# Kernel optimization log

Hardware: AMD Instinct MI355X
Metric: run time of the kernel (lower is better)

The kernel has to match this reference:

```python
import jax, jax.numpy as jnp
import numpy as np

B, N, C, H = 2, 1024, 768, 12
D = C // H
SCALE = D ** -0.5


def setup_inputs() -> dict:
    key = jax.random.key(0)
    ks = jax.random.split(key, 6)
    s = 1.0 / np.sqrt(C)
    return {
        "x": jax.random.normal(ks[0], (B, N, C), jnp.float32),
        "Wqkv": jax.random.normal(ks[1], (3 * C, C), jnp.float32) * s,   # qkv_bias=False
        "Wa": jax.random.normal(ks[2], (H, C), jnp.float32) * s,        # selective gate Linear(dim, H)
        "ba": jnp.zeros((H,), jnp.float32),
        "Wproj": jax.random.normal(ks[3], (C, C), jnp.float32) * s,
        "bproj": jnp.zeros((C,), jnp.float32),
    }


def _silu_shifted(z):
    # silu(x) + 0.5, L2-normalized over head dim (silunorm=True)
    r = jax.nn.silu(z) + 0.5
    return r / jnp.linalg.norm(r, axis=-1, keepdims=True)


def _forward(x, Wqkv, Wa, ba, Wproj, bproj):
    qkv = (x @ Wqkv.T).reshape(B, N, 3, H, D).transpose(2, 0, 3, 1, 4)  # [3,B,H,N,D]
    q = _silu_shifted(qkv[0])
    k = _silu_shifted(qkv[1])
    v = qkv[2]

    # selective forget gates: a = 1 - sigmoid(Linear(x)); torch.tensor(...) detaches -> stop_gradient
    a = jax.lax.stop_gradient(1.0 - jax.nn.sigmoid(x @ Wa.T + ba)).transpose(0, 2, 1)  # [B,H,N]
    # drop first token's gate, prepend 1 (as in the module)
    a = jnp.concatenate([jnp.ones_like(a[..., :1]), a[..., 1:]], axis=-1)

    # Causal_Mask_Selective(log(a)):
    #   A_for[i,j]  = prod_{t=j..i-1} a[t]   (j <= i)
    #   A_back[i,j] = prod_{t=i+1..j} a[t]   (j >= i)
    #   M = A_for + A_back - I
    c = jnp.cumsum(jnp.log(a), axis=-1)
    c = jnp.concatenate([jnp.zeros_like(c[..., :1]), c], axis=-1)  # [B,H,N+1], c[m] = sum log a[0..m-1]
    tri = jnp.tril(jnp.ones((N, N), bool))
    d_for = c[..., :N, None] - c[..., None, :N]      # c[i]-c[j]
    d_back = c[..., None, 1:] - c[..., 1:, None]     # c[j+1]-c[i+1]
    A_for = jnp.where(tri, jnp.exp(jnp.where(tri, d_for, 0.0)), 0.0)
    A_back = jnp.where(tri.T, jnp.exp(jnp.where(tri.T, d_back, 0.0)), 0.0)
    M = A_for + A_back - jnp.eye(N, dtype=x.dtype)

    attn = jnp.einsum('bhid,bhjd->bhij', q, k) * SCALE * M
    attn = attn / (attn.sum(axis=-1, keepdims=True) + 1e-6)  # sum-normalization, NOT softmax
    out = jnp.einsum('bhij,bhjd->bhid', attn, v).transpose(0, 2, 1, 3).reshape(B, N, C)
    return out @ Wproj.T + bproj


def reference(x, Wqkv, Wa, ba, Wproj, bproj):
    return _forward(x, Wqkv, Wa, ba, Wproj, bproj)
```

## Files before the change

### kernel.cpp

```cpp
#include <hip/hip_runtime.h>
#include <hip/hip_bf16.h>

#define BB 2
#define NN 1024
#define CC 768
#define HH 12
#define DD 64
#define SCALE_F 0.125f

typedef __attribute__((ext_vector_type(8))) __bf16 bf16x8;
typedef __attribute__((ext_vector_type(8))) unsigned short u16x8;
typedef __attribute__((ext_vector_type(4))) unsigned short u16x4;
typedef __attribute__((ext_vector_type(4))) float f32x4;

static __device__ __forceinline__ bf16x8 as_bf16x8(u16x8 v) {
  return __builtin_bit_cast(bf16x8, v);
}
static __device__ __forceinline__ unsigned short bf16u(float f) {
  __hip_bfloat16 h = __float2bfloat16(f);
  return __builtin_bit_cast(unsigned short, h);
}
static __device__ __forceinline__ float bf2f(unsigned short u) {
  unsigned int x = ((unsigned int)u) << 16;
  return __builtin_bit_cast(float, x);
}
static __device__ __forceinline__ void gload16(const void* g, void* l) {
  __builtin_amdgcn_global_load_lds(
      (const __attribute__((address_space(1))) unsigned int*)g,
      (__attribute__((address_space(3))) unsigned int*)l, 16, 0, 0);
}

__global__ __launch_bounds__(256) void packgate(
    const float* __restrict__ x, const float* __restrict__ Wa,
    const float* __restrict__ ba, float* __restrict__ loga,
    unsigned short* __restrict__ xb, int n0,
    const float* __restrict__ Wqkv, unsigned short* __restrict__ wqkvb, int n1,
    const float* __restrict__ Wproj, unsigned short* __restrict__ wprojb,
    int n2) {
  __shared__ float was[HH][CC];
  if (blockIdx.x < 512) {
    for (int i = threadIdx.x; i < HH * CC; i += 256)
      was[i / CC][i % CC] = Wa[i];
    __syncthreads();
    const int w = threadIdx.x >> 6, lane = threadIdx.x & 63;
    const int row = blockIdx.x * 4 + w;
    const int b = row >> 10, n = row & 1023;
    const float* xr = x + (size_t)row * CC;
    float xf[12];
#pragma unroll
    for (int j = 0; j < 12; j++) xf[j] = xr[lane + 64 * j];
    float myacc = 0.f;
#pragma unroll
    for (int h = 0; h < HH; h++) {
      float a = 0.f;
#pragma unroll
      for (int j = 0; j < 12; j++) a += xf[j] * was[h][lane + 64 * j];
#pragma unroll
      for (int off = 32; off >= 1; off >>= 1) a += __shfl_xor(a, off, 64);
      if (lane == h) myacc = a;
    }
    if (lane < HH) {
      float acc = myacc + ba[lane];
      float a = 1.f - 1.f / (1.f + __expf(-acc));
      float la = (n == 0) ? 0.f : log2f(a);
      loga[(b * HH + lane) * NN + n] = la;
    }
  } else {
    int i = (blockIdx.x - 512) * 256 + threadIdx.x;
    const float* s;
    unsigned short* d;
    if (i < n0) {
      s = x; d = xb;
    } else if (i < n0 + n1) {
      i -= n0; s = Wqkv; d = wqkvb;
    } else {
      i -= n0 + n1;
      if (i >= n2) return;
      s = Wproj; d = wprojb;
    }
    float4 v = ((const float4*)s)[i];
    u16x4 u = {bf16u(v.x), bf16u(v.y), bf16u(v.z), bf16u(v.w)};
    *(u16x4*)&d[i * 4] = u;
  }
}

template <int BM, int BN, bool BF16OUT>
__global__ __launch_bounds__(256) void gemm_mfma(
    const unsigned short* __restrict__ A, const unsigned short* __restrict__ W,
    const float* __restrict__ bias, void* __restrict__ outv,
    int M, int Nc, int K) {
  __shared__ unsigned short As[2][BM * 64];
  __shared__ unsigned short Ws[2][BN * 64];
  constexpr int FM = BM / 32, FN = BN / 32;
  const int row0 = blockIdx.y * BM;
  const int col0 = blockIdx.x * BN;
  const int t = threadIdx.x;
  const int w = t >> 6, lane = t & 63;
  const int lrow = lane & 15, lgrp = lane >> 4;
  const int wr = w >> 1, wc = w & 1;

  f32x4 acc[FM][FN] = {};

  auto STAGE = [&](int buf, int k0) {
#pragma unroll
    for (int i = 0; i < BM * 8 / 256; i++) {
      int idx = i * 256 + t;
      int row = idx >> 3, sl = (idx & 7) ^ (row & 7);
      gload16(A + (size_t)(row0 + row) * K + k0 + sl * 8, &As[buf][idx * 8]);
    }
#pragma unroll
    for (int i = 0; i < BN * 8 / 256; i++) {
      int idx = i * 256 + t;
      int row = idx >> 3, sl = (idx & 7) ^ (row & 7);
      gload16(W + (size_t)(col0 + row) * K + k0 + sl * 8, &Ws[buf][idx * 8]);
    }
  };

  const int NT = K / 64;
  STAGE(0, 0);
  __syncthreads();

  for (int tt = 0; tt < NT; tt++) {
    const int cur = tt & 1;
    if (tt + 1 < NT) STAGE(cur ^ 1, (tt + 1) * 64);

    bf16x8 af[FM][2], bf[FN][2];
#pragma unroll
    for (int m = 0; m < FM; m++) {
      int row = wr * (BM / 2) + m * 16 + lrow;
      const u16x8* p = (const u16x8*)&As[cur][row * 64];
#pragma unroll
      for (int hk = 0; hk < 2; hk++)
        af[m][hk] = as_bf16x8(p[(hk * 4 + lgrp) ^ (row & 7)]);
    }
#pragma unroll
    for (int n = 0; n < FN; n++) {
      int row = wc * (BN / 2) + n * 16 + lrow;
      const u16x8* p = (const u16x8*)&Ws[cur][row * 64];
#pragma unroll
      for (int hk = 0; hk < 2; hk++)
        bf[n][hk] = as_bf16x8(p[(hk * 4 + lgrp) ^ (row & 7)]);
    }
#pragma unroll
    for (int m = 0; m < FM; m++)
#pragma unroll
      for (int n = 0; n < FN; n++) {
        acc[m][n] = __builtin_amdgcn_mfma_f32_16x16x32_bf16(
            af[m][0], bf[n][0], acc[m][n], 0, 0, 0);
        acc[m][n] = __builtin_amdgcn_mfma_f32_16x16x32_bf16(
            af[m][1], bf[n][1], acc[m][n], 0, 0, 0);
      }
    __syncthreads();
  }

#pragma unroll
  for (int n = 0; n < FN; n++) {
    int col = col0 + wc * (BN / 2) + n * 16 + lrow;
    float bb = (!BF16OUT && bias) ? bias[col] : 0.f;
#pragma unroll
    for (int m = 0; m < FM; m++) {
      int rbase = row0 + wr * (BM / 2) + m * 16 + lgrp * 4;
#pragma unroll
      for (int r = 0; r < 4; r++) {
        float v = acc[m][n][r] + bb;
        if (BF16OUT)
          ((unsigned short*)outv)[(size_t)(rbase + r) * Nc + col] = bf16u(v);
        else
          ((float*)outv)[(size_t)(rbase + r) * Nc + col] = v;
      }
    }
  }
}

__global__ __launch_bounds__(256) void packscan(
    const unsigned short* __restrict__ qkvb, unsigned short* __restrict__ qp,
    unsigned short* __restrict__ kp, unsigned short* __restrict__ vt,
    const float* __restrict__ loga, float* __restrict__ c) {
  __shared__ unsigned short tile[64][65];
  if (blockIdx.x < 12288) {
    const int wid = (blockIdx.x * 256 + threadIdx.x) >> 6;
    const int lane = threadIdx.x & 63;
    int s = wid & 1;
    int rest = wid >> 1;
    int h = rest % HH;
    int n = (rest / HH) % NN;
    int b = rest / (HH * NN);
    float z = bf2f(qkvb[(((size_t)(b * NN + n) * 3 + s) * CC) + h * DD + lane]);
    float sig = 1.f / (1.f + __expf(-z));
    float r = z * sig + 0.5f;
    float ss = r * r;
#pragma unroll
    for (int off = 32; off >= 1; off >>= 1) ss += __shfl_xor(ss, off, 64);
    r *= rsqrtf(ss);
    unsigned short* dst = s ? kp : qp;
    dst[((size_t)(b * HH + h) * NN + n) * DD + lane] = bf16u(r);
  } else if (blockIdx.x < 12672) {
    const int blk = blockIdx.x - 12288;
    const int nt = blk & 15;
    const int bh = blk >> 4;
    const int b = bh / HH, h = bh % HH;
    const int n0 = nt * 64;
    const int t = threadIdx.x;
#pragma unroll
    for (int rep = 0; rep < 16; rep++) {
      int idx = rep * 256 + t;
      int nl = idx >> 6, d = idx & 63;
      tile[d][nl] =
          qkvb[((size_t)(b * NN + n0 + nl) * 3 + 2) * CC + h * DD + d];
    }
    __syncthreads();
#pragma unroll
    for (int rep = 0; rep < 16; rep++) {
      int idx = rep * 256 + t;
      int d = idx >> 6, nl = idx & 63;
      vt[((size_t)bh * DD + d) * NN + n0 + nl] = tile[d][nl];
    }
  } else if (threadIdx.x < 64) {
    const int bh = blockIdx.x - 12672;
    const int lane = threadIdx.x;
    const float4* s4 = (const float4*)(loga + (size_t)bh * NN + lane * 16);
    float v[16];
#pragma unroll
    for (int q = 0; q < 4; q++) {
      float4 tv = s4[q];
      v[q * 4 + 0] = tv.x; v[q * 4 + 1] = tv.y;
      v[q * 4 + 2] = tv.z; v[q * 4 + 3] = tv.w;
    }
    float run = 0.f;
#pragma unroll
    for (int e = 0; e < 16; e++) { run += v[e]; v[e] = run; }
    float tot = run;
#pragma unroll
    for (int off = 1; off < 64; off <<= 1) {
      float nb = __shfl_up(tot, off, 64);
      if (lane >= off) tot += nb;
    }
    float excl = tot - run;
    float* dst = c + (size_t)bh * (NN + 1);
    if (lane == 0) dst[0] = 0.f;
#pragma unroll
    for (int e = 0; e < 16; e++) dst[1 + lane * 16 + e] = v[e] + excl;
  }
}

__global__ __launch_bounds__(256) void attn_mfma(
    const unsigned short* __restrict__ qp, const unsigned short* __restrict__ kp,
    const unsigned short* __restrict__ vt, const float* __restrict__ cbuf,
    unsigned short* __restrict__ attnout) {
  __shared__ unsigned short Ks[2][64 * 64];
  __shared__ unsigned short Vs[2][64 * 64];
  __shared__ unsigned short Aw[4][16 * 64];
  __shared__ float Cw[2][64][17];
  __shared__ float Rw[2][64][5];

  const int qt2 = blockIdx.x & 31;
  const int bh = blockIdx.x >> 5;
  const int b = bh / HH, h = bh % HH;
  const int qrow0 = qt2 * 32;
  const int w = threadIdx.x >> 6;
  const int lane = threadIdx.x & 63;
  const int lrow = lane & 15;
  const int lgrp = lane >> 4;
  const int wq = w & 1;
  const int js = w >> 1;

  bf16x8 qaf[2];
  {
    const u16x8* qrow_p = (const u16x8*)(qp +
        ((size_t)bh * NN + qrow0 + wq * 16 + lrow) * DD);
#pragma unroll
    for (int hk = 0; hk < 2; hk++) qaf[hk] = as_bf16x8(qrow_p[hk * 4 + lgrp]);
  }

  const float* cbh = cbuf + (size_t)bh * (NN + 1);
  float ci[4], ci1[4];
  const int ibase = qrow0 + wq * 16 + lgrp * 4;
#pragma unroll
  for (int r = 0; r < 4; r++) {
    ci[r] = cbh[ibase + r];
    ci1[r] = cbh[ibase + r + 1];
  }

  f32x4 oacc[4] = {};
  float rs[4] = {0.f, 0.f, 0.f, 0.f};

  unsigned short* ksf = &Ks[0][0];
  unsigned short* vsf = &Vs[0][0];

  for (int t = 0; t < 8; t++) {
#pragma unroll
    for (int rep = 0; rep < 4; rep++) {
      int idx = rep * 256 + threadIdx.x;
      int buf = idx >> 9, row = (idx >> 3) & 63;
      int sl = (idx & 7) ^ (row & 7);
      int j0s = (buf * 8 + t) * 64;
      gload16(kp + ((size_t)bh * NN + j0s + row) * DD + sl * 8, ksf + idx * 8);
      gload16(vt + ((size_t)bh * DD + row) * NN + j0s + sl * 8, vsf + idx * 8);
    }
    __syncthreads();

    const int j0 = (js * 8 + t) * 64;

#pragma unroll
    for (int ct = 0; ct < 4; ct++) {
      const int jl = ct * 16 + lrow;
      const int j = j0 + jl;
      f32x4 s = {};
      const u16x8* krow_p = (const u16x8*)&Ks[js][jl * 64];
#pragma unroll
      for (int hk = 0; hk < 2; hk++) {
        bf16x8 kf = as_bf16x8(krow_p[(hk * 4 + lgrp) ^ (jl & 7)]);
        s = __builtin_amdgcn_mfma_f32_16x16x32_bf16(qaf[hk], kf, s, 0, 0, 0);
      }
      const float cj = cbh[j], cj1 = cbh[j + 1];
#pragma unroll
      for (int r = 0; r < 4; r++) {
        const int gi = ibase + r;
        float m = (gi > j) ? exp2f(ci[r] - cj)
                 : (gi < j) ? exp2f(cj1 - ci1[r]) : 1.0f;
        float av = s[r] * SCALE_F * m;
        rs[r] += av;
        int rowa = lgrp * 4 + r;
        Aw[w][rowa * 64 + (jl ^ ((rowa & 7) << 3))] = bf16u(av);
      }
    }

#pragma unroll
    for (int jh = 0; jh < 2; jh++) {
      const u16x8* arow_p = (const u16x8*)&Aw[w][lrow * 64];
      bf16x8 af = as_bf16x8(arow_p[(jh * 4 + lgrp) ^ (lrow & 7)]);
#pragma unroll
      for (int dt = 0; dt < 4; dt++) {
        const int dd = dt * 16 + lrow;
        const u16x8* vrow_p = (const u16x8*)&Vs[js][dd * 64];
        bf16x8 vf = as_bf16x8(vrow_p[(jh * 4 + lgrp) ^ (dd & 7)]);
        oacc[dt] =
            __builtin_amdgcn_mfma_f32_16x16x32_bf16(af, vf, oacc[dt], 0, 0, 0);
      }
    }
    __syncthreads();
  }

#pragma unroll
  for (int r = 0; r < 4; r++) {
#pragma unroll
    for (int off = 1; off <= 8; off <<= 1) rs[r] += __shfl_xor(rs[r], off, 64);
  }

  if (w >= 2) {
#pragma unroll
    for (int dt = 0; dt < 4; dt++)
#pragma unroll
      for (int r = 0; r < 4; r++) Cw[w - 2][lane][dt * 4 + r] = oacc[dt][r];
#pragma unroll
    for (int r = 0; r < 4; r++) Rw[w - 2][lane][r] = rs[r];
  }
  __syncthreads();
  if (w < 2) {
#pragma unroll
    for (int r = 0; r < 4; r++) {
      rs[r] += Rw[w][lane][r];
      rs[r] = 1.f / (rs[r] + 1e-6f);
    }
#pragma unroll
    for (int dt = 0; dt < 4; dt++) {
#pragma unroll
      for (int r = 0; r < 4; r++) {
        const int gi = ibase + r;
        float val = (oacc[dt][r] + Cw[w][lane][dt * 4 + r]) * rs[r];
        attnout[((size_t)b * NN + gi) * CC + h * DD + dt * 16 + lrow] =
            bf16u(val);
      }
    }
  }
}

extern "C" void kernel_launch(void* const* d_in, const int* in_sizes, int n_in,
                              void* d_out, int out_size, void* d_ws,
                              size_t ws_size, hipStream_t stream) {
  const float* x = (const float*)d_in[0];
  const float* Wqkv = (const float*)d_in[1];
  const float* Wa = (const float*)d_in[2];
  const float* ba = (const float*)d_in[3];
  const float* Wproj = (const float*)d_in[4];
  const float* bproj = (const float*)d_in[5];
  float* out = (float*)d_out;

  unsigned short* qkvb = (unsigned short*)d_ws;
  float* loga = (float*)(qkvb + (size_t)BB * NN * 3 * CC);
  float* cbuf = loga + (size_t)BB * HH * NN;
  unsigned short* qp = (unsigned short*)(cbuf + (size_t)BB * HH * (NN + 1));
  unsigned short* kp = qp + (size_t)BB * HH * NN * DD;
  unsigned short* vt = kp + (size_t)BB * HH * NN * DD;
  unsigned short* xb = vt + (size_t)BB * HH * NN * DD;
  unsigned short* wqkvb = xb + (size_t)BB * NN * CC;
  unsigned short* wprojb = wqkvb + (size_t)3 * CC * CC;
  unsigned short* attnoutb = qkvb;

  const int n0 = BB * NN * CC / 4, n1 = 3 * CC * CC / 4, n2 = CC * CC / 4;

  packgate<<<512 + (n0 + n1 + n2 + 255) / 256, 256, 0, stream>>>(
      x, Wa, ba, loga, xb, n0, Wqkv, wqkvb, n1, Wproj, wprojb, n2);
  {
    dim3 grid(3 * CC / 128, BB * NN / 64);
    gemm_mfma<64, 128, true><<<grid, 256, 0, stream>>>(
        xb, wqkvb, nullptr, qkvb, BB * NN, 3 * CC, CC);
  }
  packscan<<<12696, 256, 0, stream>>>(qkvb, qp, kp, vt, loga, cbuf);
  attn_mfma<<<BB * HH * (NN / 32), 256, 0, stream>>>(qp, kp, vt, cbuf,
                                                     attnoutb);
  {
    dim3 grid(CC / 64, BB * NN / 64);
    gemm_mfma<64, 64, false><<<grid, 256, 0, stream>>>(
        attnoutb, wprojb, bproj, out, BB * NN, CC, CC);
  }
}
```

Measured before the change: 146.3 us.

## Fuse silu-norm and V transpose into QKV GEMM epilogue, scan in attention

Removes the separate packscan kernel. The QKV GEMM epilogue now applies the shifted-SiLU and L2 normalization to Q/K, using a cross-lane shuffle over head-dim columns, and writes V transposed directly. The cumulative log-gate scan moves into each attention block and is stored in shared memory, with LDS regions aliased to fit. This drops one launch and a full bf16 qkv round trip through global memory. In exchange the GEMM epilogue does strided scattered stores and every attention block recomputes the scan redundantly.

Result: faster. 128.7 us (-12.0%).

```diff
diff --git a/kernel.cpp b/kernel.cpp
--- a/kernel.cpp
+++ b/kernel.cpp
@@ -19,10 +19,6 @@
 static __device__ __forceinline__ unsigned short bf16u(float f) {
   __hip_bfloat16 h = __float2bfloat16(f);
   return __builtin_bit_cast(unsigned short, h);
-}
-static __device__ __forceinline__ float bf2f(unsigned short u) {
-  unsigned int x = ((unsigned int)u) << 16;
-  return __builtin_bit_cast(float, x);
 }
 static __device__ __forceinline__ void gload16(const void* g, void* l) {
   __builtin_amdgcn_global_load_lds(
@@ -84,11 +80,12 @@
   }
 }
 
-template <int BM, int BN, bool BF16OUT>
+template <int BM, int BN, int EPI>
 __global__ __launch_bounds__(256) void gemm_mfma(
     const unsigned short* __restrict__ A, const unsigned short* __restrict__ W,
     const float* __restrict__ bias, void* __restrict__ outv,
-    int M, int Nc, int K) {
+    unsigned short* __restrict__ qp, unsigned short* __restrict__ kp,
+    unsigned short* __restrict__ vtp, int M, int Nc, int K) {
   __shared__ unsigned short As[2][BM * 64];
   __shared__ unsigned short Ws[2][BN * 64];
   constexpr int FM = BM / 32, FN = BN / 32;
@@ -153,105 +150,77 @@
     __syncthreads();
   }
 
-#pragma unroll
-  for (int n = 0; n < FN; n++) {
-    int col = col0 + wc * (BN / 2) + n * 16 + lrow;
-    float bb = (!BF16OUT && bias) ? bias[col] : 0.f;
-#pragma unroll
-    for (int m = 0; m < FM; m++) {
-      int rbase = row0 + wr * (BM / 2) + m * 16 + lgrp * 4;
-#pragma unroll
-      for (int r = 0; r < 4; r++) {
-        float v = acc[m][n][r] + bb;
-        if (BF16OUT)
-          ((unsigned short*)outv)[(size_t)(rbase + r) * Nc + col] = bf16u(v);
-        else
-          ((float*)outv)[(size_t)(rbase + r) * Nc + col] = v;
-      }
-    }
-  }
-}
-
-__global__ __launch_bounds__(256) void packscan(
-    const unsigned short* __restrict__ qkvb, unsigned short* __restrict__ qp,
-    unsigned short* __restrict__ kp, unsigned short* __restrict__ vt,
-    const float* __restrict__ loga, float* __restrict__ c) {
-  __shared__ unsigned short tile[64][65];
-  if (blockIdx.x < 12288) {
-    const int wid = (blockIdx.x * 256 + threadIdx.x) >> 6;
-    const int lane = threadIdx.x & 63;
-    int s = wid & 1;
-    int rest = wid >> 1;
-    int h = rest % HH;
-    int n = (rest / HH) % NN;
-    int b = rest / (HH * NN);
-    float z = bf2f(qkvb[(((size_t)(b * NN + n) * 3 + s) * CC) + h * DD + lane]);
-    float sig = 1.f / (1.f + __expf(-z));
-    float r = z * sig + 0.5f;
-    float ss = r * r;
-#pragma unroll
-    for (int off = 32; off >= 1; off >>= 1) ss += __shfl_xor(ss, off, 64);
-    r *= rsqrtf(ss);
-    unsigned short* dst = s ? kp : qp;
-    dst[((size_t)(b * HH + h) * NN + n) * DD + lane] = bf16u(r);
-  } else if (blockIdx.x < 12672) {
-    const int blk = blockIdx.x - 12288;
-    const int nt = blk & 15;
-    const int bh = blk >> 4;
-    const int b = bh / HH, h = bh % HH;
-    const int n0 = nt * 64;
-    const int t = threadIdx.x;
-#pragma unroll
-    for (int rep = 0; rep < 16; rep++) {
-      int idx = rep * 256 + t;
-      int nl = idx >> 6, d = idx & 63;
-      tile[d][nl] =
-          qkvb[((size_t)(b * NN + n0 + nl) * 3 + 2) * CC + h * DD + d];
-    }
-    __syncthreads();
-#pragma unroll
-    for (int rep = 0; rep < 16; rep++) {
-      int idx = rep * 256 + t;
-      int d = idx >> 6, nl = idx & 63;
-      vt[((size_t)bh * DD + d) * NN + n0 + nl] = tile[d][nl];
-    }
-  } else if (threadIdx.x < 64) {
-    const int bh = blockIdx.x - 12672;
-    const int lane = threadIdx.x;
-    const float4* s4 = (const float4*)(loga + (size_t)bh * NN + lane * 16);
-    float v[16];
-#pragma unroll
-    for (int q = 0; q < 4; q++) {
-      float4 tv = s4[q];
-      v[q * 4 + 0] = tv.x; v[q * 4 + 1] = tv.y;
-      v[q * 4 + 2] = tv.z; v[q * 4 + 3] = tv.w;
-    }
-    float run = 0.f;
-#pragma unroll
-    for (int e = 0; e < 16; e++) { run += v[e]; v[e] = run; }
-    float tot = run;
-#pragma unroll
-    for (int off = 1; off < 64; off <<= 1) {
-      float nb = __shfl_up(tot, off, 64);
-      if (lane >= off) tot += nb;
-    }
-    float excl = tot - run;
-    float* dst = c + (size_t)bh * (NN + 1);
-    if (lane == 0) dst[0] = 0.f;
-#pragma unroll
-    for (int e = 0; e < 16; e++) dst[1 + lane * 16 + e] = v[e] + excl;
+  if constexpr (EPI == 0) {
+#pragma unroll
+    for (int n = 0; n < FN; n++) {
+      int col = col0 + wc * (BN / 2) + n * 16 + lrow;
+      float bb = bias ? bias[col] : 0.f;
+#pragma unroll
+      for (int m = 0; m < FM; m++) {
+        int rbase = row0 + wr * (BM / 2) + m * 16 + lgrp * 4;
+#pragma unroll
+        for (int r = 0; r < 4; r++)
+          ((float*)outv)[(size_t)(rbase + r) * Nc + col] = acc[m][n][r] + bb;
+      }
+    }
+  } else {
+    const int sec = col0 / CC;
+    const int h = ((col0 % CC) >> 6) + wc;
+    const int rb = row0 + wr * (BM / 2);
+    const int b = rb >> 10;
+    const int nbase = rb & (NN - 1);
+    const size_t bh = (size_t)b * HH + h;
+    if (sec < 2) {
+      unsigned short* dst = sec ? kp : qp;
+#pragma unroll
+      for (int m = 0; m < FM; m++) {
+#pragma unroll
+        for (int r = 0; r < 4; r++) {
+          float sil[FN];
+          float ss = 0.f;
+#pragma unroll
+          for (int n = 0; n < FN; n++) {
+            float v = acc[m][n][r];
+            float s = v / (1.f + __expf(-v)) + 0.5f;
+            sil[n] = s;
+            ss += s * s;
+          }
+#pragma unroll
+          for (int off = 1; off <= 8; off <<= 1) ss += __shfl_xor(ss, off, 64);
+          float rn = rsqrtf(ss);
+          int nn = nbase + m * 16 + lgrp * 4 + r;
+#pragma unroll
+          for (int n = 0; n < FN; n++)
+            dst[(bh * NN + nn) * DD + n * 16 + lrow] = bf16u(sil[n] * rn);
+        }
+      }
+    } else {
+#pragma unroll
+      for (int m = 0; m < FM; m++) {
+#pragma unroll
+        for (int n = 0; n < FN; n++) {
+          int d = n * 16 + lrow;
+          int nn0 = nbase + m * 16 + lgrp * 4;
+          u16x4 pkt = {bf16u(acc[m][n][0]), bf16u(acc[m][n][1]),
+                       bf16u(acc[m][n][2]), bf16u(acc[m][n][3])};
+          *(u16x4*)&vtp[(bh * DD + d) * NN + nn0] = pkt;
+        }
+      }
+    }
   }
 }
 
 __global__ __launch_bounds__(256) void attn_mfma(
     const unsigned short* __restrict__ qp, const unsigned short* __restrict__ kp,
-    const unsigned short* __restrict__ vt, const float* __restrict__ cbuf,
+    const unsigned short* __restrict__ vt, const float* __restrict__ loga,
     unsigned short* __restrict__ attnout) {
-  __shared__ unsigned short Ks[2][64 * 64];
-  __shared__ unsigned short Vs[2][64 * 64];
-  __shared__ unsigned short Aw[4][16 * 64];
-  __shared__ float Cw[2][64][17];
-  __shared__ float Rw[2][64][5];
+  __shared__ __align__(16) unsigned char smem[45072];
+  unsigned short* Ks = (unsigned short*)smem;
+  unsigned short* Vs = (unsigned short*)(smem + 16384);
+  unsigned short* AwB = (unsigned short*)(smem + 32768);
+  float* cls = (float*)(smem + 40960);
+  float* CwB = (float*)smem;
+  float* RwB = (float*)(smem + 8704);
 
   const int qt2 = blockIdx.x & 31;
   const int bh = blockIdx.x >> 5;
@@ -264,6 +233,30 @@
   const int wq = w & 1;
   const int js = w >> 1;
 
+  if (w == 0) {
+    const float4* s4 = (const float4*)(loga + (size_t)bh * NN + lane * 16);
+    float v[16];
+#pragma unroll
+    for (int q = 0; q < 4; q++) {
+      float4 tv = s4[q];
+      v[q * 4 + 0] = tv.x; v[q * 4 + 1] = tv.y;
+      v[q * 4 + 2] = tv.z; v[q * 4 + 3] = tv.w;
+    }
+    float run = 0.f;
+#pragma unroll
+    for (int e = 0; e < 16; e++) { run += v[e]; v[e] = run; }
+    float tot = run;
+#pragma unroll
+    for (int off = 1; off < 64; off <<= 1) {
+      float nb = __shfl_up(tot, off, 64);
+      if (lane >= off) tot += nb;
+    }
+    float excl = tot - run;
+    if (lane == 0) cls[0] = 0.f;
+#pragma unroll
+    for (int e = 0; e < 16; e++) cls[1 + lane * 16 + e] = v[e] + excl;
+  }
+
   bf16x8 qaf[2];
   {
     const u16x8* qrow_p = (const u16x8*)(qp +
@@ -272,20 +265,10 @@
     for (int hk = 0; hk < 2; hk++) qaf[hk] = as_bf16x8(qrow_p[hk * 4 + lgrp]);
   }
 
-  const float* cbh = cbuf + (size_t)bh * (NN + 1);
+  const int ibase = qrow0 + wq * 16 + lgrp * 4;
   float ci[4], ci1[4];
-  const int ibase = qrow0 + wq * 16 + lgrp * 4;
-#pragma unroll
-  for (int r = 0; r < 4; r++) {
-    ci[r] = cbh[ibase + r];
-    ci1[r] = cbh[ibase + r + 1];
-  }
-
   f32x4 oacc[4] = {};
   float rs[4] = {0.f, 0.f, 0.f, 0.f};
-
-  unsigned short* ksf = &Ks[0][0];
-  unsigned short* vsf = &Vs[0][0];
 
   for (int t = 0; t < 8; t++) {
 #pragma unroll
@@ -294,10 +277,17 @@
       int buf = idx >> 9, row = (idx >> 3) & 63;
       int sl = (idx & 7) ^ (row & 7);
       int j0s = (buf * 8 + t) * 64;
-      gload16(kp + ((size_t)bh * NN + j0s + row) * DD + sl * 8, ksf + idx * 8);
-      gload16(vt + ((size_t)bh * DD + row) * NN + j0s + sl * 8, vsf + idx * 8);
+      gload16(kp + ((size_t)bh * NN + j0s + row) * DD + sl * 8, Ks + idx * 8);
+      gload16(vt + ((size_t)bh * DD + row) * NN + j0s + sl * 8, Vs + idx * 8);
     }
     __syncthreads();
+    if (t == 0) {
+#pragma unroll
+      for (int r = 0; r < 4; r++) {
+        ci[r] = cls[ibase + r];
+        ci1[r] = cls[ibase + r + 1];
+      }
+    }
 
     const int j0 = (js * 8 + t) * 64;
 
@@ -306,13 +296,13 @@
       const int jl = ct * 16 + lrow;
       const int j = j0 + jl;
       f32x4 s = {};
-      const u16x8* krow_p = (const u16x8*)&Ks[js][jl * 64];
+      const u16x8* krow_p = (const u16x8*)(Ks + js * 4096 + jl * 64);
 #pragma unroll
       for (int hk = 0; hk < 2; hk++) {
         bf16x8 kf = as_bf16x8(krow_p[(hk * 4 + lgrp) ^ (jl & 7)]);
         s = __builtin_amdgcn_mfma_f32_16x16x32_bf16(qaf[hk], kf, s, 0, 0, 0);
       }
-      const float cj = cbh[j], cj1 = cbh[j + 1];
+      const float cj = cls[j], cj1 = cls[j + 1];
 #pragma unroll
       for (int r = 0; r < 4; r++) {
         const int gi = ibase + r;
@@ -321,18 +311,18 @@
         float av = s[r] * SCALE_F * m;
         rs[r] += av;
         int rowa = lgrp * 4 + r;
-        Aw[w][rowa * 64 + (jl ^ ((rowa & 7) << 3))] = bf16u(av);
+        AwB[w * 1024 + rowa * 64 + (jl ^ ((rowa & 7) << 3))] = bf16u(av);
       }
     }
 
 #pragma unroll
     for (int jh = 0; jh < 2; jh++) {
-      const u16x8* arow_p = (const u16x8*)&Aw[w][lrow * 64];
+      const u16x8* arow_p = (const u16x8*)(AwB + w * 1024 + lrow * 64);
       bf16x8 af = as_bf16x8(arow_p[(jh * 4 + lgrp) ^ (lrow & 7)]);
 #pragma unroll
       for (int dt = 0; dt < 4; dt++) {
         const int dd = dt * 16 + lrow;
-        const u16x8* vrow_p = (const u16x8*)&Vs[js][dd * 64];
+        const u16x8* vrow_p = (const u16x8*)(Vs + js * 4096 + dd * 64);
         bf16x8 vf = as_bf16x8(vrow_p[(jh * 4 + lgrp) ^ (dd & 7)]);
         oacc[dt] =
             __builtin_amdgcn_mfma_f32_16x16x32_bf16(af, vf, oacc[dt], 0, 0, 0);
@@ -351,15 +341,16 @@
 #pragma unroll
     for (int dt = 0; dt < 4; dt++)
 #pragma unroll
-      for (int r = 0; r < 4; r++) Cw[w - 2][lane][dt * 4 + r] = oacc[dt][r];
-#pragma unroll
-    for (int r = 0; r < 4; r++) Rw[w - 2][lane][r] = rs[r];
+      for (int r = 0; r < 4; r++)
+        CwB[((w - 2) * 64 + lane) * 17 + dt * 4 + r] = oacc[dt][r];
+#pragma unroll
+    for (int r = 0; r < 4; r++) RwB[((w - 2) * 64 + lane) * 5 + r] = rs[r];
   }
   __syncthreads();
   if (w < 2) {
 #pragma unroll
     for (int r = 0; r < 4; r++) {
-      rs[r] += Rw[w][lane][r];
+      rs[r] += RwB[(w * 64 + lane) * 5 + r];
       rs[r] = 1.f / (rs[r] + 1e-6f);
     }
 #pragma unroll
@@ -367,7 +358,8 @@
 #pragma unroll
       for (int r = 0; r < 4; r++) {
         const int gi = ibase + r;
-        float val = (oacc[dt][r] + Cw[w][lane][dt * 4 + r]) * rs[r];
+        float val =
+            (oacc[dt][r] + CwB[(w * 64 + lane) * 17 + dt * 4 + r]) * rs[r];
         attnout[((size_t)b * NN + gi) * CC + h * DD + dt * 16 + lrow] =
             bf16u(val);
       }
@@ -386,16 +378,14 @@
   const float* bproj = (const float*)d_in[5];
   float* out = (float*)d_out;
 
-  unsigned short* qkvb = (unsigned short*)d_ws;
-  float* loga = (float*)(qkvb + (size_t)BB * NN * 3 * CC);
-  float* cbuf = loga + (size_t)BB * HH * NN;
-  unsigned short* qp = (unsigned short*)(cbuf + (size_t)BB * HH * (NN + 1));
+  unsigned short* obuf = (unsigned short*)d_ws;
+  float* loga = (float*)(obuf + (size_t)BB * NN * CC);
+  unsigned short* qp = (unsigned short*)(loga + (size_t)BB * HH * NN);
   unsigned short* kp = qp + (size_t)BB * HH * NN * DD;
   unsigned short* vt = kp + (size_t)BB * HH * NN * DD;
   unsigned short* xb = vt + (size_t)BB * HH * NN * DD;
   unsigned short* wqkvb = xb + (size_t)BB * NN * CC;
   unsigned short* wprojb = wqkvb + (size_t)3 * CC * CC;
-  unsigned short* attnoutb = qkvb;
 
   const int n0 = BB * NN * CC / 4, n1 = 3 * CC * CC / 4, n2 = CC * CC / 4;
 
@@ -403,15 +393,13 @@
       x, Wa, ba, loga, xb, n0, Wqkv, wqkvb, n1, Wproj, wprojb, n2);
   {
     dim3 grid(3 * CC / 128, BB * NN / 64);
-    gemm_mfma<64, 128, true><<<grid, 256, 0, stream>>>(
-        xb, wqkvb, nullptr, qkvb, BB * NN, 3 * CC, CC);
-  }
-  packscan<<<12696, 256, 0, stream>>>(qkvb, qp, kp, vt, loga, cbuf);
-  attn_mfma<<<BB * HH * (NN / 32), 256, 0, stream>>>(qp, kp, vt, cbuf,
-                                                     attnoutb);
+    gemm_mfma<64, 128, 2><<<grid, 256, 0, stream>>>(
+        xb, wqkvb, nullptr, nullptr, qp, kp, vt, BB * NN, 3 * CC, CC);
+  }
+  attn_mfma<<<BB * HH * (NN / 32), 256, 0, stream>>>(qp, kp, vt, loga, obuf);
   {
     dim3 grid(CC / 64, BB * NN / 64);
-    gemm_mfma<64, 64, false><<<grid, 256, 0, stream>>>(
-        attnoutb, wprojb, bproj, out, BB * NN, CC, CC);
-  }
-}
+    gemm_mfma<64, 64, 0><<<grid, 256, 0, stream>>>(
+        obuf, wprojb, bproj, out, nullptr, nullptr, nullptr, BB * NN, CC, CC);
+  }
+}
```
